# Performance work log

Hardware: AMD Instinct MI355X
Metric: run time of the kernel (lower is better)

Reference implementation:

```python
import jax, jax.numpy as jnp
import numpy as np

Bsz, L, D, N = 2, 2048, 1024, 16
LN_EPS = 1e-5


def setup_inputs() -> dict:
    key = jax.random.key(0)
    ks = jax.random.split(key, 5)
    # A_log initialized as in the module: -log(arange(1, N+1)) broadcast over D
    A_log = -jnp.broadcast_to(jnp.log(jnp.arange(1, N + 1, dtype=jnp.float32))[None, :], (D, N))
    return {
        "x": jax.random.normal(ks[0], (Bsz, L, D), jnp.float32),
        "W_dt": jax.random.normal(ks[1], (D, D), jnp.float32) * 0.02,
        "b_dt": jnp.zeros((D,), jnp.float32),
        "W_B": jax.random.normal(ks[2], (N, D), jnp.float32) * 0.02,
        "W_C": jax.random.normal(ks[3], (N, D), jnp.float32) * 0.02,
        "D_param": jnp.ones((D,), jnp.float32),
        "A_log": A_log,
        "gamma": jnp.ones((D,), jnp.float32),
        "beta": jnp.zeros((D,), jnp.float32),
    }


def reference(x, W_dt, b_dt, W_B, W_C, D_param, A_log, gamma, beta):
    residual = x
    # LayerNorm (biased variance, eps=1e-5)
    mu = jnp.mean(x, axis=-1, keepdims=True)
    var = jnp.var(x, axis=-1, keepdims=True)
    xn = (x - mu) * jax.lax.rsqrt(var + LN_EPS) * gamma + beta

    dt = jax.nn.softplus(xn @ W_dt.T + b_dt)          # (B, L, D)
    A = -jnp.exp(A_log)                                # (D, N)
    B_in = xn @ W_B.T                                  # (B, L, N)
    C_in = xn @ W_C.T                                  # (B, L, N)

    A_bar = jnp.exp(dt[..., None] * A)                 # (B, L, D, N)
    # B_bar[t] * x[t] fused: dt * B_in * xn -> (B, L, D, N)
    Bx = dt[..., None] * B_in[:, :, None, :] * xn[..., None]

    def step(h, inputs):
        a_t, bx_t, c_t = inputs                        # (B,D,N), (B,D,N), (B,N)
        h = a_t * h + bx_t                             # (B, D, N)
        y_t = jnp.einsum('bn,bdn->bd', c_t, h)         # (B, D)
        return h, y_t

    h0 = jnp.zeros((x.shape[0], D, N), x.dtype)
    _, ys = jax.lax.scan(
        step, h0,
        (jnp.transpose(A_bar, (1, 0, 2, 3)),
         jnp.transpose(Bx, (1, 0, 2, 3)),
         jnp.transpose(C_in, (1, 0, 2))))
    y = jnp.transpose(ys, (1, 0, 2)) + D_param * residual
    return y
```

## Files before the change

kernel.cpp:

```cpp
#include <hip/hip_runtime.h>
#include <cstddef>

#define Bsz 2
#define Lr  2048
#define Dr  1024
#define Nr  16
#define M_ROWS (Bsz*Lr)
#define NPAD   1088
#define CHUNK  32
#define NCH    (Lr/CHUNK)

#define BM 64
#define BN 64
#define BK 32
#define NK (Dr/BK)

typedef __attribute__((ext_vector_type(8))) __bf16 bf16x8;
typedef __attribute__((ext_vector_type(4))) float floatx4;

__device__ __forceinline__ unsigned short f2bf(float f) {
    unsigned u = __float_as_uint(f);
    u += 0x7fffu + ((u >> 16) & 1u);
    return (unsigned short)(u >> 16);
}

__device__ __forceinline__ float bf2f(unsigned short u) {
    return __uint_as_float(((unsigned)u) << 16);
}

__device__ __forceinline__ float softplus_f(float x) {
    if (x > 0.f) return x + __logf(1.f + __expf(-x));
    return __logf(1.f + __expf(x));
}

__device__ __forceinline__ void gload_lds16(const unsigned short* g, unsigned short* l) {
    __builtin_amdgcn_global_load_lds((const __attribute__((address_space(1))) void*)g,
                                     (__attribute__((address_space(3))) void*)l, 16, 0, 0);
}

__global__ __launch_bounds__(256) void ln_pack_kernel(const float* __restrict__ x,
                                                      const float* __restrict__ gamma,
                                                      const float* __restrict__ beta,
                                                      unsigned short* __restrict__ xnb,
                                                      const float* __restrict__ Wdt,
                                                      const float* __restrict__ WB,
                                                      const float* __restrict__ WC,
                                                      unsigned short* __restrict__ Wcat) {
    if (blockIdx.x >= M_ROWS) {
        int i = (blockIdx.x - M_ROWS) * 256 + threadIdx.x;
        int row = i >> 10;
        int col = i & 1023;
        float v;
        if (row < Dr)                 v = Wdt[i];
        else if (row < Dr + Nr)       v = WB[(row - Dr) * Dr + col];
        else if (row < Dr + 2*Nr)     v = WC[(row - Dr - Nr) * Dr + col];
        else                          v = 0.f;
        Wcat[i] = f2bf(v);
        return;
    }
    int row = blockIdx.x;
    int tid = threadIdx.x;
    const float4* xr = (const float4*)(x + (size_t)row * Dr);
    float4 v = xr[tid];
    float s  = v.x + v.y + v.z + v.w;
    float ss = v.x*v.x + v.y*v.y + v.z*v.z + v.w*v.w;
    #pragma unroll
    for (int off = 32; off > 0; off >>= 1) {
        s  += __shfl_down(s, off);
        ss += __shfl_down(ss, off);
    }
    __shared__ float red[8];
    int wid = tid >> 6;
    if ((tid & 63) == 0) { red[wid*2] = s; red[wid*2+1] = ss; }
    __syncthreads();
    if (tid == 0) {
        float S = 0.f, SS = 0.f;
        #pragma unroll
        for (int w = 0; w < 4; w++) { S += red[w*2]; SS += red[w*2+1]; }
        float mu  = S * (1.f/Dr);
        float var = SS * (1.f/Dr) - mu*mu;
        red[0] = mu;
        red[1] = rsqrtf(var + 1e-5f);
    }
    __syncthreads();
    float mu = red[0], rs = red[1];
    float4 g = ((const float4*)gamma)[tid], bt = ((const float4*)beta)[tid];
    float4 o;
    o.x = (v.x - mu) * rs * g.x + bt.x;
    o.y = (v.y - mu) * rs * g.y + bt.y;
    o.z = (v.z - mu) * rs * g.z + bt.z;
    o.w = (v.w - mu) * rs * g.w + bt.w;
    ushort4 ob;
    ob.x = f2bf(o.x); ob.y = f2bf(o.y); ob.z = f2bf(o.z); ob.w = f2bf(o.w);
    ((ushort4*)(xnb + (size_t)row * Dr))[tid] = ob;
}

__global__ __launch_bounds__(256) void gemm_kernel(const unsigned short* __restrict__ xnb,
                                                   const unsigned short* __restrict__ w,
                                                   const float* __restrict__ b_dt,
                                                   float* __restrict__ dt,
                                                   float* __restrict__ bin,
                                                   float* __restrict__ cin) {
    __shared__ unsigned short As[BM * BK];
    __shared__ unsigned short Bs[BN * BK];
    int tid  = threadIdx.x;
    int wave = tid >> 6;
    int lane = tid & 63;
    int lm   = lane & 15;
    int quad = lane >> 4;
    int bid  = blockIdx.x;
    int xcd  = bid & 7;
    int j0   = bid >> 3;
    int nt   = j0 % 17;
    int mt   = (j0 / 17) * 8 + xcd;
    int Mb = mt * BM;
    int Nb = nt * BN;
    int wm = (wave >> 1) * 32;
    int wn = (wave & 1)  * 32;
    int koff = (mt + nt) & (NK - 1);

    int srow = tid >> 2, sch = tid & 3;
    const unsigned short* Ag = xnb + (size_t)(Mb + srow) * Dr + sch * 8;
    const unsigned short* Bg = w   + (size_t)(Nb + srow) * Dr + sch * 8;
    unsigned short* Al = &As[tid * 8];
    unsigned short* Bl = &Bs[tid * 8];
    const unsigned short* Ar = &As[(wm + lm) * BK + quad * 8];
    const unsigned short* Br = &Bs[(wn + lm) * BK + quad * 8];

    floatx4 acc[2][2] = {};

    for (int kk = 0; kk < NK; kk++) {
        int k0 = ((kk + koff) & (NK - 1)) * BK;
        gload_lds16(Ag + k0, Al);
        gload_lds16(Bg + k0, Bl);
        __syncthreads();
        bf16x8 a0 = *(const bf16x8*)(Ar);
        bf16x8 a1 = *(const bf16x8*)(Ar + 16 * BK);
        bf16x8 b0 = *(const bf16x8*)(Br);
        bf16x8 b1 = *(const bf16x8*)(Br + 16 * BK);
        acc[0][0] = __builtin_amdgcn_mfma_f32_16x16x32_bf16(a0, b0, acc[0][0], 0, 0, 0);
        acc[0][1] = __builtin_amdgcn_mfma_f32_16x16x32_bf16(a0, b1, acc[0][1], 0, 0, 0);
        acc[1][0] = __builtin_amdgcn_mfma_f32_16x16x32_bf16(a1, b0, acc[1][0], 0, 0, 0);
        acc[1][1] = __builtin_amdgcn_mfma_f32_16x16x32_bf16(a1, b1, acc[1][1], 0, 0, 0);
        __syncthreads();
    }

    #pragma unroll
    for (int i = 0; i < 2; i++) {
        int grow0 = Mb + wm + i * 16 + quad * 4;
        #pragma unroll
        for (int jj = 0; jj < 2; jj++) {
            int gcol = Nb + wn + jj * 16 + lm;
            #pragma unroll
            for (int r = 0; r < 4; r++) {
                float v = acc[i][jj][r];
                int row = grow0 + r;
                if (gcol < Dr) {
                    dt[(size_t)row * Dr + gcol] = softplus_f(v + b_dt[gcol]);
                } else if (gcol < Dr + Nr) {
                    bin[(size_t)row * Nr + (gcol - Dr)] = v;
                } else if (gcol < Dr + 2*Nr) {
                    cin[(size_t)row * Nr + (gcol - Dr - Nr)] = v;
                }
            }
        }
    }
}

__global__ __launch_bounds__(256) void scan1_kernel(const float* __restrict__ dt,
                                                    const unsigned short* __restrict__ xnb,
                                                    const float* __restrict__ bin,
                                                    const float* __restrict__ A_log,
                                                    float* __restrict__ Pws,
                                                    float* __restrict__ hendws) {
    int d  = blockIdx.x * 256 + threadIdx.x;
    int ch = blockIdx.y;
    int b  = blockIdx.z;
    int l0 = ch * CHUNK;
    size_t rowbase = (size_t)b * Lr + l0;

    float ac[16];
    #pragma unroll
    for (int i = 0; i < 4; i++) {
        float4 t = ((const float4*)(A_log + (size_t)d * Nr))[i];
        ac[i*4+0] = -__expf(t.x);
        ac[i*4+1] = -__expf(t.y);
        ac[i*4+2] = -__expf(t.z);
        ac[i*4+3] = -__expf(t.w);
    }

    __shared__ float lb[CHUNK * Nr];
    for (int i = threadIdx.x; i < CHUNK * Nr; i += 256)
        lb[i] = bin[rowbase * Nr + i];
    __syncthreads();

    float h[16];
    #pragma unroll
    for (int n = 0; n < 16; n++) h[n] = 0.f;
    float S = 0.f;

    const float* dtp          = dt  + rowbase * Dr + d;
    const unsigned short* xp  = xnb + rowbase * Dr + d;

    for (int tb = 0; tb < CHUNK; tb += 4) {
        float dt4[4], xv4[4];
        #pragma unroll
        for (int u = 0; u < 4; u++) {
            dt4[u] = dtp[(tb + u) * Dr];
            xv4[u] = bf2f(xp[(tb + u) * Dr]);
        }
        #pragma unroll
        for (int u = 0; u < 4; u++) {
            float dtv = dt4[u];
            float xv  = xv4[u];
            S += dtv;
            float cm = dtv * xv;
            const float* br = lb + (tb + u) * Nr;
            float4 b0 = *(const float4*)(br);
            float4 b1 = *(const float4*)(br + 4);
            float4 b2 = *(const float4*)(br + 8);
            float4 b3 = *(const float4*)(br + 12);
            h[0]  = __expf(dtv*ac[0])  * h[0]  + cm * b0.x;
            h[1]  = __expf(dtv*ac[1])  * h[1]  + cm * b0.y;
            h[2]  = __expf(dtv*ac[2])  * h[2]  + cm * b0.z;
            h[3]  = __expf(dtv*ac[3])  * h[3]  + cm * b0.w;
            h[4]  = __expf(dtv*ac[4])  * h[4]  + cm * b1.x;
            h[5]  = __expf(dtv*ac[5])  * h[5]  + cm * b1.y;
            h[6]  = __expf(dtv*ac[6])  * h[6]  + cm * b1.z;
            h[7]  = __expf(dtv*ac[7])  * h[7]  + cm * b1.w;
            h[8]  = __expf(dtv*ac[8])  * h[8]  + cm * b2.x;
            h[9]  = __expf(dtv*ac[9])  * h[9]  + cm * b2.y;
            h[10] = __expf(dtv*ac[10]) * h[10] + cm * b2.z;
            h[11] = __expf(dtv*ac[11]) * h[11] + cm * b2.w;
            h[12] = __expf(dtv*ac[12]) * h[12] + cm * b3.x;
            h[13] = __expf(dtv*ac[13]) * h[13] + cm * b3.y;
            h[14] = __expf(dtv*ac[14]) * h[14] + cm * b3.z;
            h[15] = __expf(dtv*ac[15]) * h[15] + cm * b3.w;
        }
    }

    size_t obase = ((size_t)(b * NCH + ch) * Nr) * Dr + d;
    #pragma unroll
    for (int n = 0; n < 16; n++) {
        Pws[obase + (size_t)n * Dr]    = __expf(S * ac[n]);
        hendws[obase + (size_t)n * Dr] = h[n];
    }
}

__global__ __launch_bounds__(256) void combine_kernel(const float* __restrict__ Pws,
                                                      const float* __restrict__ hendws,
                                                      float* __restrict__ hinws) {
    int id = blockIdx.x * 256 + threadIdx.x;
    int b  = id >> 14;
    int dn = id & 16383;
    size_t base = ((size_t)b * NCH) * (Nr * Dr) + dn;
    float hin = 0.f;
    for (int cb = 0; cb < NCH; cb += 4) {
        float p[4], he[4];
        #pragma unroll
        for (int u = 0; u < 4; u++) {
            size_t idx = base + (size_t)(cb + u) * (Nr * Dr);
            p[u]  = Pws[idx];
            he[u] = hendws[idx];
        }
        #pragma unroll
        for (int u = 0; u < 4; u++) {
            size_t idx = base + (size_t)(cb + u) * (Nr * Dr);
            hinws[idx] = hin;
            hin = p[u] * hin + he[u];
        }
    }
}

__global__ __launch_bounds__(256) void scan2_kernel(const float* __restrict__ dt,
                                                    const unsigned short* __restrict__ xnb,
                                                    const float* __restrict__ bin,
                                                    const float* __restrict__ cin,
                                                    const float* __restrict__ A_log,
                                                    const float* __restrict__ hinws,
                                                    const float* __restrict__ x,
                                                    const float* __restrict__ Dp,
                                                    float* __restrict__ out) {
    int d  = blockIdx.x * 256 + threadIdx.x;
    int ch = blockIdx.y;
    int b  = blockIdx.z;
    int l0 = ch * CHUNK;
    size_t rowbase = (size_t)b * Lr + l0;

    float ac[16];
    #pragma unroll
    for (int i = 0; i < 4; i++) {
        float4 t = ((const float4*)(A_log + (size_t)d * Nr))[i];
        ac[i*4+0] = -__expf(t.x);
        ac[i*4+1] = -__expf(t.y);
        ac[i*4+2] = -__expf(t.z);
        ac[i*4+3] = -__expf(t.w);
    }

    __shared__ float lb[CHUNK * Nr];
    __shared__ float lc[CHUNK * Nr];
    for (int i = threadIdx.x; i < CHUNK * Nr; i += 256) {
        lb[i] = bin[rowbase * Nr + i];
        lc[i] = cin[rowbase * Nr + i];
    }
    __syncthreads();

    size_t obase = ((size_t)(b * NCH + ch) * Nr) * Dr + d;
    float h[16];
    #pragma unroll
    for (int n = 0; n < 16; n++) h[n] = hinws[obase + (size_t)n * Dr];

    float dp = Dp[d];
    const float* dtp         = dt  + rowbase * Dr + d;
    const unsigned short* xp = xnb + rowbase * Dr + d;
    const float* xr          = x   + rowbase * Dr + d;
    float* op                = out + rowbase * Dr + d;

    for (int tb = 0; tb < CHUNK; tb += 4) {
        float dt4[4], xv4[4], xr4[4];
        #pragma unroll
        for (int u = 0; u < 4; u++) {
            dt4[u] = dtp[(tb + u) * Dr];
            xv4[u] = bf2f(xp[(tb + u) * Dr]);
            xr4[u] = xr[(tb + u) * Dr];
        }
        #pragma unroll
        for (int u = 0; u < 4; u++) {
            float dtv = dt4[u];
            float xv  = xv4[u];
            float cm = dtv * xv;
            const float* br = lb + (tb + u) * Nr;
            const float* cr = lc + (tb + u) * Nr;
            float4 b0 = *(const float4*)(br);
            float4 b1 = *(const float4*)(br + 4);
            float4 b2 = *(const float4*)(br + 8);
            float4 b3 = *(const float4*)(br + 12);
            float4 c0 = *(const float4*)(cr);
            float4 c1 = *(const float4*)(cr + 4);
            float4 c2 = *(const float4*)(cr + 8);
            float4 c3 = *(const float4*)(cr + 12);
            float y = 0.f;
            h[0]  = __expf(dtv*ac[0])  * h[0]  + cm * b0.x;  y += c0.x * h[0];
            h[1]  = __expf(dtv*ac[1])  * h[1]  + cm * b0.y;  y += c0.y * h[1];
            h[2]  = __expf(dtv*ac[2])  * h[2]  + cm * b0.z;  y += c0.z * h[2];
            h[3]  = __expf(dtv*ac[3])  * h[3]  + cm * b0.w;  y += c0.w * h[3];
            h[4]  = __expf(dtv*ac[4])  * h[4]  + cm * b1.x;  y += c1.x * h[4];
            h[5]  = __expf(dtv*ac[5])  * h[5]  + cm * b1.y;  y += c1.y * h[5];
            h[6]  = __expf(dtv*ac[6])  * h[6]  + cm * b1.z;  y += c1.z * h[6];
            h[7]  = __expf(dtv*ac[7])  * h[7]  + cm * b1.w;  y += c1.w * h[7];
            h[8]  = __expf(dtv*ac[8])  * h[8]  + cm * b2.x;  y += c2.x * h[8];
            h[9]  = __expf(dtv*ac[9])  * h[9]  + cm * b2.y;  y += c2.y * h[9];
            h[10] = __expf(dtv*ac[10]) * h[10] + cm * b2.z;  y += c2.z * h[10];
            h[11] = __expf(dtv*ac[11]) * h[11] + cm * b2.w;  y += c2.w * h[11];
            h[12] = __expf(dtv*ac[12]) * h[12] + cm * b3.x;  y += c3.x * h[12];
            h[13] = __expf(dtv*ac[13]) * h[13] + cm * b3.y;  y += c3.y * h[13];
            h[14] = __expf(dtv*ac[14]) * h[14] + cm * b3.z;  y += c3.z * h[14];
            h[15] = __expf(dtv*ac[15]) * h[15] + cm * b3.w;  y += c3.w * h[15];
            op[(tb + u) * Dr] = y + dp * xr4[u];
        }
    }
}

extern "C" void kernel_launch(void* const* d_in, const int* in_sizes, int n_in,
                              void* d_out, int out_size, void* d_ws, size_t ws_size,
                              hipStream_t stream) {
    const float* x      = (const float*)d_in[0];
    const float* W_dt   = (const float*)d_in[1];
    const float* b_dt   = (const float*)d_in[2];
    const float* W_B    = (const float*)d_in[3];
    const float* W_C    = (const float*)d_in[4];
    const float* Dparam = (const float*)d_in[5];
    const float* A_log  = (const float*)d_in[6];
    const float* gamma  = (const float*)d_in[7];
    const float* beta   = (const float*)d_in[8];
    float* out = (float*)d_out;

    char* ws = (char*)d_ws;
    unsigned short* xnb  = (unsigned short*)(ws);
    unsigned short* wcat = (unsigned short*)(ws + 8388608);
    float*          dt   = (float*)(ws + 10616832);
    float*          bin  = (float*)(ws + 27394048);
    float*          cin  = (float*)(ws + 27656192);
    float*          Pws  = (float*)(ws + 27918336);
    float*          hend = (float*)(ws + 36306944);
    float*          hin  = (float*)(ws + 44695552);

    ln_pack_kernel<<<M_ROWS + (NPAD * Dr) / 256, 256, 0, stream>>>(
        x, gamma, beta, xnb, W_dt, W_B, W_C, wcat);
    gemm_kernel<<<(M_ROWS / BM) * (NPAD / BN), 256, 0, stream>>>(xnb, wcat, b_dt, dt, bin, cin);
    dim3 sgrid(Dr / 256, NCH, Bsz);
    scan1_kernel<<<sgrid, 256, 0, stream>>>(dt, xnb, bin, A_log, Pws, hend);
    combine_kernel<<<(Bsz * Dr * Nr) / 256, 256, 0, stream>>>(Pws, hend, hin);
    scan2_kernel<<<sgrid, 256, 0, stream>>>(dt, xnb, bin, cin, A_log, hin, x, Dparam, out);
}
```

Baseline: 159.4 us.

## Fuse chunked scan passes into cooperative kernel, store dt as bf16, widen GEMM K tile

Replaces the three scan launches (chunk scan, cross-chunk combine, output scan) with one cooperative kernel. It uses grid syncs and keeps each thread's dt and xn chunk values in registers, so the second pass does not reload them from memory. dt is now stored as bf16, which halves its write and read traffic but lowers its precision. The GEMM K tile grows to 64 with an XOR-swizzled LDS layout to cut loop iterations and bank conflicts. The old three-kernel path stays as a fallback when occupancy or the cooperative launch does not allow the fused kernel.

Result: no change. 159.6 us (+0.1%).

```diff
diff --git a/kernel.cpp b/kernel.cpp
--- a/kernel.cpp
+++ b/kernel.cpp
@@ -1,5 +1,8 @@
 #include <hip/hip_runtime.h>
+#include <hip/hip_cooperative_groups.h>
 #include <cstddef>
+
+namespace cg = cooperative_groups;
 
 #define Bsz 2
 #define Lr  2048
@@ -12,7 +15,7 @@
 
 #define BM 64
 #define BN 64
-#define BK 32
+#define BK 64
 #define NK (Dr/BK)
 
 typedef __attribute__((ext_vector_type(8))) __bf16 bf16x8;
@@ -98,7 +101,7 @@
 __global__ __launch_bounds__(256) void gemm_kernel(const unsigned short* __restrict__ xnb,
                                                    const unsigned short* __restrict__ w,
                                                    const float* __restrict__ b_dt,
-                                                   float* __restrict__ dt,
+                                                   unsigned short* __restrict__ dt,
                                                    float* __restrict__ bin,
                                                    float* __restrict__ cin) {
     __shared__ unsigned short As[BM * BK];
@@ -119,29 +122,40 @@
     int wn = (wave & 1)  * 32;
     int koff = (mt + nt) & (NK - 1);
 
-    int srow = tid >> 2, sch = tid & 3;
-    const unsigned short* Ag = xnb + (size_t)(Mb + srow) * Dr + sch * 8;
-    const unsigned short* Bg = w   + (size_t)(Nb + srow) * Dr + sch * 8;
-    unsigned short* Al = &As[tid * 8];
-    unsigned short* Bl = &Bs[tid * 8];
-    const unsigned short* Ar = &As[(wm + lm) * BK + quad * 8];
-    const unsigned short* Br = &Bs[(wn + lm) * BK + quad * 8];
+    int r0 = tid >> 3,        cg0 = (tid & 7) ^ (r0 & 7);
+    int r1 = (tid + 256) >> 3, cg1 = ((tid + 256) & 7) ^ (r1 & 7);
+    const unsigned short* Ag0 = xnb + (size_t)(Mb + r0) * Dr + cg0 * 8;
+    const unsigned short* Ag1 = xnb + (size_t)(Mb + r1) * Dr + cg1 * 8;
+    const unsigned short* Bg0 = w   + (size_t)(Nb + r0) * Dr + cg0 * 8;
+    const unsigned short* Bg1 = w   + (size_t)(Nb + r1) * Dr + cg1 * 8;
+    unsigned short* Al0 = &As[(size_t)tid * 8];
+    unsigned short* Al1 = &As[(size_t)(tid + 256) * 8];
+    unsigned short* Bl0 = &Bs[(size_t)tid * 8];
+    unsigned short* Bl1 = &Bs[(size_t)(tid + 256) * 8];
 
     floatx4 acc[2][2] = {};
 
     for (int kk = 0; kk < NK; kk++) {
         int k0 = ((kk + koff) & (NK - 1)) * BK;
-        gload_lds16(Ag + k0, Al);
-        gload_lds16(Bg + k0, Bl);
+        gload_lds16(Ag0 + k0, Al0);
+        gload_lds16(Ag1 + k0, Al1);
+        gload_lds16(Bg0 + k0, Bl0);
+        gload_lds16(Bg1 + k0, Bl1);
         __syncthreads();
-        bf16x8 a0 = *(const bf16x8*)(Ar);
-        bf16x8 a1 = *(const bf16x8*)(Ar + 16 * BK);
-        bf16x8 b0 = *(const bf16x8*)(Br);
-        bf16x8 b1 = *(const bf16x8*)(Br + 16 * BK);
-        acc[0][0] = __builtin_amdgcn_mfma_f32_16x16x32_bf16(a0, b0, acc[0][0], 0, 0, 0);
-        acc[0][1] = __builtin_amdgcn_mfma_f32_16x16x32_bf16(a0, b1, acc[0][1], 0, 0, 0);
-        acc[1][0] = __builtin_amdgcn_mfma_f32_16x16x32_bf16(a1, b0, acc[1][0], 0, 0, 0);
-        acc[1][1] = __builtin_amdgcn_mfma_f32_16x16x32_bf16(a1, b1, acc[1][1], 0, 0, 0);
+        #pragma unroll
+        for (int s = 0; s < 2; s++) {
+            int ra0 = wm + lm, ra1 = wm + 16 + lm;
+            int rb0 = wn + lm, rb1 = wn + 16 + lm;
+            int cg = s * 4 + quad;
+            bf16x8 a0 = *(const bf16x8*)&As[ra0 * BK + ((cg ^ (ra0 & 7)) * 8)];
+            bf16x8 a1 = *(const bf16x8*)&As[ra1 * BK + ((cg ^ (ra1 & 7)) * 8)];
+            bf16x8 b0 = *(const bf16x8*)&Bs[rb0 * BK + ((cg ^ (rb0 & 7)) * 8)];
+            bf16x8 b1 = *(const bf16x8*)&Bs[rb1 * BK + ((cg ^ (rb1 & 7)) * 8)];
+            acc[0][0] = __builtin_amdgcn_mfma_f32_16x16x32_bf16(a0, b0, acc[0][0], 0, 0, 0);
+            acc[0][1] = __builtin_amdgcn_mfma_f32_16x16x32_bf16(a0, b1, acc[0][1], 0, 0, 0);
+            acc[1][0] = __builtin_amdgcn_mfma_f32_16x16x32_bf16(a1, b0, acc[1][0], 0, 0, 0);
+            acc[1][1] = __builtin_amdgcn_mfma_f32_16x16x32_bf16(a1, b1, acc[1][1], 0, 0, 0);
+        }
         __syncthreads();
     }
 
@@ -156,7 +170,7 @@
                 float v = acc[i][jj][r];
                 int row = grow0 + r;
                 if (gcol < Dr) {
-                    dt[(size_t)row * Dr + gcol] = softplus_f(v + b_dt[gcol]);
+                    dt[(size_t)row * Dr + gcol] = f2bf(softplus_f(v + b_dt[gcol]));
                 } else if (gcol < Dr + Nr) {
                     bin[(size_t)row * Nr + (gcol - Dr)] = v;
                 } else if (gcol < Dr + 2*Nr) {
@@ -167,7 +181,142 @@
     }
 }
 
-__global__ __launch_bounds__(256) void scan1_kernel(const float* __restrict__ dt,
+__global__ __launch_bounds__(256, 2) void scan_fused_kernel(
+        const unsigned short* __restrict__ dtb,
+        const unsigned short* __restrict__ xnb,
+        const float* __restrict__ bin,
+        const float* __restrict__ cin,
+        const float* __restrict__ A_log,
+        const float* __restrict__ x,
+        const float* __restrict__ Dp,
+        float* __restrict__ Pws,
+        float* __restrict__ hendws,
+        float* __restrict__ hinws,
+        float* __restrict__ out) {
+    cg::grid_group grid = cg::this_grid();
+    int tid  = threadIdx.x;
+    int bid  = blockIdx.x;
+    int dblk = bid & 3;
+    int ch   = (bid >> 2) & 63;
+    int b    = bid >> 8;
+    int d    = dblk * 256 + tid;
+    size_t rowbase = (size_t)b * Lr + ch * CHUNK;
+
+    float ac[16];
+    #pragma unroll
+    for (int i = 0; i < 4; i++) {
+        float4 t = ((const float4*)(A_log + (size_t)d * Nr))[i];
+        ac[i*4+0] = -__expf(t.x);
+        ac[i*4+1] = -__expf(t.y);
+        ac[i*4+2] = -__expf(t.z);
+        ac[i*4+3] = -__expf(t.w);
+    }
+
+    __shared__ float lb[CHUNK * Nr];
+    __shared__ float lc[CHUNK * Nr];
+    for (int i = tid; i < CHUNK * Nr; i += 256) {
+        lb[i] = bin[rowbase * Nr + i];
+        lc[i] = cin[rowbase * Nr + i];
+    }
+    __syncthreads();
+
+    float dtv[CHUNK], xv[CHUNK];
+    {
+        const unsigned short* dtp = dtb + rowbase * Dr + d;
+        const unsigned short* xp  = xnb + rowbase * Dr + d;
+        #pragma unroll
+        for (int t = 0; t < CHUNK; t++) {
+            dtv[t] = bf2f(dtp[(size_t)t * Dr]);
+            xv[t]  = bf2f(xp[(size_t)t * Dr]);
+        }
+    }
+
+    float h[16];
+    #pragma unroll
+    for (int n = 0; n < 16; n++) h[n] = 0.f;
+    float S = 0.f;
+    #pragma unroll
+    for (int t = 0; t < CHUNK; t++) {
+        float dv = dtv[t];
+        S += dv;
+        float cm = dv * xv[t];
+        const float4* br4 = (const float4*)(lb + t * Nr);
+        float4 q0 = br4[0], q1 = br4[1], q2 = br4[2], q3 = br4[3];
+        float bb[16] = {q0.x,q0.y,q0.z,q0.w, q1.x,q1.y,q1.z,q1.w,
+                        q2.x,q2.y,q2.z,q2.w, q3.x,q3.y,q3.z,q3.w};
+        #pragma unroll
+        for (int n = 0; n < 16; n++)
+            h[n] = __expf(dv * ac[n]) * h[n] + cm * bb[n];
+    }
+    size_t obase = ((size_t)(b * NCH + ch) * Nr) * Dr + d;
+    #pragma unroll
+    for (int n = 0; n < 16; n++) {
+        Pws[obase + (size_t)n * Dr]    = __expf(S * ac[n]);
+        hendws[obase + (size_t)n * Dr] = h[n];
+    }
+
+    grid.sync();
+
+    if (bid < 128) {
+        int id = bid * 256 + tid;
+        int b2 = id >> 14;
+        int dn = id & 16383;
+        size_t base = ((size_t)b2 * NCH) * (Nr * Dr) + dn;
+        float hin = 0.f;
+        for (int cb = 0; cb < NCH; cb += 4) {
+            float p[4], he[4];
+            #pragma unroll
+            for (int u = 0; u < 4; u++) {
+                size_t idx = base + (size_t)(cb + u) * (Nr * Dr);
+                p[u]  = Pws[idx];
+                he[u] = hendws[idx];
+            }
+            #pragma unroll
+            for (int u = 0; u < 4; u++) {
+                size_t idx = base + (size_t)(cb + u) * (Nr * Dr);
+                hinws[idx] = hin;
+                hin = p[u] * hin + he[u];
+            }
+        }
+    }
+
+    grid.sync();
+
+    #pragma unroll
+    for (int n = 0; n < 16; n++) h[n] = hinws[obase + (size_t)n * Dr];
+    float dp = Dp[d];
+    const float* xr = x   + rowbase * Dr + d;
+    float* op       = out + rowbase * Dr + d;
+
+    for (int tb = 0; tb < CHUNK; tb += 4) {
+        float xr4[4];
+        #pragma unroll
+        for (int u = 0; u < 4; u++) xr4[u] = xr[(size_t)(tb + u) * Dr];
+        #pragma unroll
+        for (int u = 0; u < 4; u++) {
+            int t = tb + u;
+            float dv = dtv[t];
+            float cm = dv * xv[t];
+            const float4* br4 = (const float4*)(lb + t * Nr);
+            const float4* cr4 = (const float4*)(lc + t * Nr);
+            float4 q0 = br4[0], q1 = br4[1], q2 = br4[2], q3 = br4[3];
+            float4 r0 = cr4[0], r1 = cr4[1], r2 = cr4[2], r3 = cr4[3];
+            float bb[16] = {q0.x,q0.y,q0.z,q0.w, q1.x,q1.y,q1.z,q1.w,
+                            q2.x,q2.y,q2.z,q2.w, q3.x,q3.y,q3.z,q3.w};
+            float cc[16] = {r0.x,r0.y,r0.z,r0.w, r1.x,r1.y,r1.z,r1.w,
+                            r2.x,r2.y,r2.z,r2.w, r3.x,r3.y,r3.z,r3.w};
+            float y = 0.f;
+            #pragma unroll
+            for (int n = 0; n < 16; n++) {
+                h[n] = __expf(dv * ac[n]) * h[n] + cm * bb[n];
+                y += cc[n] * h[n];
+            }
+            op[(size_t)t * Dr] = y + dp * xr4[u];
+        }
+    }
+}
+
+__global__ __launch_bounds__(256) void scan1_kernel(const unsigned short* __restrict__ dtb,
                                                     const unsigned short* __restrict__ xnb,
                                                     const float* __restrict__ bin,
                                                     const float* __restrict__ A_log,
@@ -176,8 +325,7 @@
     int d  = blockIdx.x * 256 + threadIdx.x;
     int ch = blockIdx.y;
     int b  = blockIdx.z;
-    int l0 = ch * CHUNK;
-    size_t rowbase = (size_t)b * Lr + l0;
+    size_t rowbase = (size_t)b * Lr + ch * CHUNK;
 
     float ac[16];
     #pragma unroll
@@ -199,43 +347,28 @@
     for (int n = 0; n < 16; n++) h[n] = 0.f;
     float S = 0.f;
 
-    const float* dtp          = dt  + rowbase * Dr + d;
+    const unsigned short* dtp = dtb + rowbase * Dr + d;
     const unsigned short* xp  = xnb + rowbase * Dr + d;
 
     for (int tb = 0; tb < CHUNK; tb += 4) {
         float dt4[4], xv4[4];
         #pragma unroll
         for (int u = 0; u < 4; u++) {
-            dt4[u] = dtp[(tb + u) * Dr];
-            xv4[u] = bf2f(xp[(tb + u) * Dr]);
-        }
-        #pragma unroll
-        for (int u = 0; u < 4; u++) {
-            float dtv = dt4[u];
-            float xv  = xv4[u];
-            S += dtv;
-            float cm = dtv * xv;
-            const float* br = lb + (tb + u) * Nr;
-            float4 b0 = *(const float4*)(br);
-            float4 b1 = *(const float4*)(br + 4);
-            float4 b2 = *(const float4*)(br + 8);
-            float4 b3 = *(const float4*)(br + 12);
-            h[0]  = __expf(dtv*ac[0])  * h[0]  + cm * b0.x;
-            h[1]  = __expf(dtv*ac[1])  * h[1]  + cm * b0.y;
-            h[2]  = __expf(dtv*ac[2])  * h[2]  + cm * b0.z;
-            h[3]  = __expf(dtv*ac[3])  * h[3]  + cm * b0.w;
-            h[4]  = __expf(dtv*ac[4])  * h[4]  + cm * b1.x;
-            h[5]  = __expf(dtv*ac[5])  * h[5]  + cm * b1.y;
-            h[6]  = __expf(dtv*ac[6])  * h[6]  + cm * b1.z;
-            h[7]  = __expf(dtv*ac[7])  * h[7]  + cm * b1.w;
-            h[8]  = __expf(dtv*ac[8])  * h[8]  + cm * b2.x;
-            h[9]  = __expf(dtv*ac[9])  * h[9]  + cm * b2.y;
-            h[10] = __expf(dtv*ac[10]) * h[10] + cm * b2.z;
-            h[11] = __expf(dtv*ac[11]) * h[11] + cm * b2.w;
-            h[12] = __expf(dtv*ac[12]) * h[12] + cm * b3.x;
-            h[13] = __expf(dtv*ac[13]) * h[13] + cm * b3.y;
-            h[14] = __expf(dtv*ac[14]) * h[14] + cm * b3.z;
-            h[15] = __expf(dtv*ac[15]) * h[15] + cm * b3.w;
+            dt4[u] = bf2f(dtp[(size_t)(tb + u) * Dr]);
+            xv4[u] = bf2f(xp[(size_t)(tb + u) * Dr]);
+        }
+        #pragma unroll
+        for (int u = 0; u < 4; u++) {
+            float dv = dt4[u];
+            S += dv;
+            float cm = dv * xv4[u];
+            const float4* br4 = (const float4*)(lb + (tb + u) * Nr);
+            float4 q0 = br4[0], q1 = br4[1], q2 = br4[2], q3 = br4[3];
+            float bb[16] = {q0.x,q0.y,q0.z,q0.w, q1.x,q1.y,q1.z,q1.w,
+                            q2.x,q2.y,q2.z,q2.w, q3.x,q3.y,q3.z,q3.w};
+            #pragma unroll
+            for (int n = 0; n < 16; n++)
+                h[n] = __expf(dv * ac[n]) * h[n] + cm * bb[n];
         }
     }
 
@@ -272,7 +405,7 @@
     }
 }
 
-__global__ __launch_bounds__(256) void scan2_kernel(const float* __restrict__ dt,
+__global__ __launch_bounds__(256) void scan2_kernel(const unsigned short* __restrict__ dtb,
                                                     const unsigned short* __restrict__ xnb,
                                                     const float* __restrict__ bin,
                                                     const float* __restrict__ cin,
@@ -284,8 +417,7 @@
     int d  = blockIdx.x * 256 + threadIdx.x;
     int ch = blockIdx.y;
     int b  = blockIdx.z;
-    int l0 = ch * CHUNK;
-    size_t rowbase = (size_t)b * Lr + l0;
+    size_t rowbase = (size_t)b * Lr + ch * CHUNK;
 
     float ac[16];
     #pragma unroll
@@ -311,52 +443,38 @@
     for (int n = 0; n < 16; n++) h[n] = hinws[obase + (size_t)n * Dr];
 
     float dp = Dp[d];
-    const float* dtp         = dt  + rowbase * Dr + d;
-    const unsigned short* xp = xnb + rowbase * Dr + d;
-    const float* xr          = x   + rowbase * Dr + d;
-    float* op                = out + rowbase * Dr + d;
+    const unsigned short* dtp = dtb + rowbase * Dr + d;
+    const unsigned short* xp  = xnb + rowbase * Dr + d;
+    const float* xr           = x   + rowbase * Dr + d;
+    float* op                 = out + rowbase * Dr + d;
 
     for (int tb = 0; tb < CHUNK; tb += 4) {
         float dt4[4], xv4[4], xr4[4];
         #pragma unroll
         for (int u = 0; u < 4; u++) {
-            dt4[u] = dtp[(tb + u) * Dr];
-            xv4[u] = bf2f(xp[(tb + u) * Dr]);
-            xr4[u] = xr[(tb + u) * Dr];
-        }
-        #pragma unroll
-        for (int u = 0; u < 4; u++) {
-            float dtv = dt4[u];
-            float xv  = xv4[u];
-            float cm = dtv * xv;
-            const float* br = lb + (tb + u) * Nr;
-            const float* cr = lc + (tb + u) * Nr;
-            float4 b0 = *(const float4*)(br);
-            float4 b1 = *(const float4*)(br + 4);
-            float4 b2 = *(const float4*)(br + 8);
-            float4 b3 = *(const float4*)(br + 12);
-            float4 c0 = *(const float4*)(cr);
-            float4 c1 = *(const float4*)(cr + 4);
-            float4 c2 = *(const float4*)(cr + 8);
-            float4 c3 = *(const float4*)(cr + 12);
+            dt4[u] = bf2f(dtp[(size_t)(tb + u) * Dr]);
+            xv4[u] = bf2f(xp[(size_t)(tb + u) * Dr]);
+            xr4[u] = xr[(size_t)(tb + u) * Dr];
+        }
+        #pragma unroll
+        for (int u = 0; u < 4; u++) {
+            float dv = dt4[u];
+            float cm = dv * xv4[u];
+            const float4* br4 = (const float4*)(lb + (tb + u) * Nr);
+            const float4* cr4 = (const float4*)(lc + (tb + u) * Nr);
+            float4 q0 = br4[0], q1 = br4[1], q2 = br4[2], q3 = br4[3];
+            float4 r0 = cr4[0], r1 = cr4[1], r2 = cr4[2], r3 = cr4[3];
+            float bb[16] = {q0.x,q0.y,q0.z,q0.w, q1.x,q1.y,q1.z,q1.w,
+                            q2.x,q2.y,q2.z,q2.w, q3.x,q3.y,q3.z,q3.w};
+            float cc[16] = {r0.x,r0.y,r0.z,r0.w, r1.x,r1.y,r1.z,r1.w,
+                            r2.x,r2.y,r2.z,r2.w, r3.x,r3.y,r3.z,r3.w};
             float y = 0.f;
-            h[0]  = __expf(dtv*ac[0])  * h[0]  + cm * b0.x;  y += c0.x * h[0];
-            h[1]  = __expf(dtv*ac[1])  * h[1]  + cm * b0.y;  y += c0.y * h[1];
-            h[2]  = __expf(dtv*ac[2])  * h[2]  + cm * b0.z;  y += c0.z * h[2];
-            h[3]  = __expf(dtv*ac[3])  * h[3]  + cm * b0.w;  y += c0.w * h[3];
-            h[4]  = __expf(dtv*ac[4])  * h[4]  + cm * b1.x;  y += c1.x * h[4];
-            h[5]  = __expf(dtv*ac[5])  * h[5]  + cm * b1.y;  y += c1.y * h[5];
-            h[6]  = __expf(dtv*ac[6])  * h[6]  + cm * b1.z;  y += c1.z * h[6];
-            h[7]  = __expf(dtv*ac[7])  * h[7]  + cm * b1.w;  y += c1.w * h[7];
-            h[8]  = __expf(dtv*ac[8])  * h[8]  + cm * b2.x;  y += c2.x * h[8];
-            h[9]  = __expf(dtv*ac[9])  * h[9]  + cm * b2.y;  y += c2.y * h[9];
-            h[10] = __expf(dtv*ac[10]) * h[10] + cm * b2.z;  y += c2.z * h[10];
-            h[11] = __expf(dtv*ac[11]) * h[11] + cm * b2.w;  y += c2.w * h[11];
-            h[12] = __expf(dtv*ac[12]) * h[12] + cm * b3.x;  y += c3.x * h[12];
-            h[13] = __expf(dtv*ac[13]) * h[13] + cm * b3.y;  y += c3.y * h[13];
-            h[14] = __expf(dtv*ac[14]) * h[14] + cm * b3.z;  y += c3.z * h[14];
-            h[15] = __expf(dtv*ac[15]) * h[15] + cm * b3.w;  y += c3.w * h[15];
-            op[(tb + u) * Dr] = y + dp * xr4[u];
+            #pragma unroll
+            for (int n = 0; n < 16; n++) {
+                h[n] = __expf(dv * ac[n]) * h[n] + cm * bb[n];
+                y += cc[n] * h[n];
+            }
+            op[(size_t)(tb + u) * Dr] = y + dp * xr4[u];
         }
     }
 }
@@ -378,18 +496,35 @@
     char* ws = (char*)d_ws;
     unsigned short* xnb  = (unsigned short*)(ws);
     unsigned short* wcat = (unsigned short*)(ws + 8388608);
-    float*          dt   = (float*)(ws + 10616832);
-    float*          bin  = (float*)(ws + 27394048);
-    float*          cin  = (float*)(ws + 27656192);
-    float*          Pws  = (float*)(ws + 27918336);
-    float*          hend = (float*)(ws + 36306944);
-    float*          hin  = (float*)(ws + 44695552);
+    unsigned short* dtb  = (unsigned short*)(ws + 10616832);
+    float*          bin  = (float*)(ws + 19005440);
+    float*          cin  = (float*)(ws + 19267584);
+    float*          Pws  = (float*)(ws + 19529728);
+    float*          hend = (float*)(ws + 27918336);
+    float*          hin  = (float*)(ws + 36306944);
 
     ln_pack_kernel<<<M_ROWS + (NPAD * Dr) / 256, 256, 0, stream>>>(
         x, gamma, beta, xnb, W_dt, W_B, W_C, wcat);
-    gemm_kernel<<<(M_ROWS / BM) * (NPAD / BN), 256, 0, stream>>>(xnb, wcat, b_dt, dt, bin, cin);
-    dim3 sgrid(Dr / 256, NCH, Bsz);
-    scan1_kernel<<<sgrid, 256, 0, stream>>>(dt, xnb, bin, A_log, Pws, hend);
-    combine_kernel<<<(Bsz * Dr * Nr) / 256, 256, 0, stream>>>(Pws, hend, hin);
-    scan2_kernel<<<sgrid, 256, 0, stream>>>(dt, xnb, bin, cin, A_log, hin, x, Dparam, out);
-}
+    gemm_kernel<<<(M_ROWS / BM) * (NPAD / BN), 256, 0, stream>>>(xnb, wcat, b_dt, dtb, bin, cin);
+
+    int maxBlk = 0;
+    hipError_t qerr = hipOccupancyMaxActiveBlocksPerMultiprocessor(
+        &maxBlk, (const void*)scan_fused_kernel, 256, 0);
+    bool coop_done = false;
+    if (qerr == hipSuccess && maxBlk >= 2) {
+        void* args[] = {
+            (void*)&dtb, (void*)&xnb, (void*)&bin, (void*)&cin, (void*)&A_log,
+            (void*)&x, (void*)&Dparam, (void*)&Pws, (void*)&hend, (void*)&hin, (void*)&out
+        };
+        hipError_t e = hipLaunchCooperativeKernel((const void*)scan_fused_kernel,
+                                                  dim3(512), dim3(256),
+                                                  args, 0, stream);
+        coop_done = (e == hipSuccess);
+    }
+    if (!coop_done) {
+        dim3 sgrid(Dr / 256, NCH, Bsz);
+        scan1_kernel<<<sgrid, 256, 0, stream>>>(dtb, xnb, bin, A_log, Pws, hend);
+        combine_kernel<<<(Bsz * Dr * Nr) / 256, 256, 0, stream>>>(Pws, hend, hin);
+        scan2_kernel<<<sgrid, 256, 0, stream>>>(dtb, xnb, bin, cin, A_log, hin, x, Dparam, out);
+    }
+}
```
